# Performance work log

Measured on AMD Instinct MI355X. Metric: run time of the kernel, lower is better.

The kernel has to match this reference:

```python
import jax, jax.numpy as jnp
import numpy as np

KS, PH, PW, SH, SW = 3, 1, 1, 1, 1


def setup_inputs() -> dict:
    key = jax.random.key(0)
    k1, k2, k3 = jax.random.split(key, 3)
    bs, p_in, H, W = 8, 64, 64, 64
    p_out = 64
    vs = KS * KS + 1
    x = jax.random.normal(k1, (bs, p_in, H, W), dtype=jnp.float32)
    # kaiming-uniform-like init scale for filters (fan_in = p_in*vs*vs)
    fan_in = p_in * vs * vs
    bound = float(np.sqrt(6.0 / fan_in))
    filters = jax.random.uniform(k2, (p_out, p_in, vs, vs), dtype=jnp.float32,
                                 minval=-bound, maxval=bound)
    biases = jax.random.uniform(k3, (p_out,), dtype=jnp.float32, minval=-1.0, maxval=1.0)
    return {"x": x, "filters": filters, "biases": biases}


def reference(x, filters, biases):
    # x: (bs, p_in, H, W); filters: (p_out, p_in, vs, vs); biases: (p_out,)
    bs, p_in = x.shape[0], x.shape[1]
    p_out = filters.shape[0]
    vs = KS * KS + 1
    # Extract ks x ks patches -> (bs, p_in*ks*ks, Ho, Wo), feature dim ordered (C, kh, kw)
    patches = jax.lax.conv_general_dilated_patches(
        x, filter_shape=(KS, KS), window_strides=(SH, SW),
        padding=[(PH, PH), (PW, PW)])
    Ho, Wo = patches.shape[-2], patches.shape[-1]
    P = patches.reshape(bs, p_in, KS * KS, Ho, Wo)
    # Prepend constant 1 -> augmented patch vector s of length vs (matches torch cat(ones, spot))
    ones = jnp.ones((bs, p_in, 1, Ho, Wo), dtype=x.dtype)
    S = jnp.concatenate([ones, P], axis=2)            # (bs, p_in, vs, Ho, Wo)
    # Move pixels to a single leading dim: (M, p_in, vs) with M = bs*Ho*Wo
    S = S.transpose(0, 3, 4, 1, 2).reshape(bs * Ho * Wo, p_in, vs)
    # Per-pixel, per-channel outer product s s^T: (M, p_in, vs, vs)
    Q = S[:, :, :, None] * S[:, :, None, :]
    # Quadratic form contraction with filters as one GEMM:
    # out[m, o] = sum_{c,i,j} Q[m,c,i,j] * filters[o,c,i,j]
    out = Q.reshape(bs * Ho * Wo, p_in * vs * vs) @ filters.reshape(p_out, -1).T
    out = out + biases[None, :]
    return out.reshape(bs, Ho, Wo, p_out).transpose(0, 3, 1, 2)
```

## Files before the change

kernel.cpp:

```cpp
#include <hip/hip_runtime.h>
#include <stdint.h>

#define HH 64
#define WW 64
#define PIN 64
#define POUT 64
#define NFEAT 54
#define SEGB 16384
#define NSEG 27

typedef _Float16 half8 __attribute__((ext_vector_type(8)));
typedef _Float16 half4 __attribute__((ext_vector_type(4)));
typedef float f32x4 __attribute__((ext_vector_type(4)));
typedef float f32x16 __attribute__((ext_vector_type(16)));

__device__ constexpr int KT[54] = {0,0,0,0,0,0,0,0,0, 1,1,1,1,1,1,1,1,1, 2,2,2,2,2,2,2,2,
                                   3,3,3,3,3,3,3, 4,4,4,4,4,4, 5,5,5,5,5, 6,6,6,6, 7,7,7, 8,8, 9};
__device__ constexpr int LT[54] = {1,2,3,4,5,6,7,8,9, 1,2,3,4,5,6,7,8,9, 2,3,4,5,6,7,8,9,
                                   3,4,5,6,7,8,9, 4,5,6,7,8,9, 5,6,7,8,9, 6,7,8,9, 7,8,9, 8,9, 9};

__global__ __launch_bounds__(256) void prep_filters(
    const float* __restrict__ f, const float* __restrict__ bias,
    _Float16* __restrict__ fprep, float* __restrict__ fconst) {
    __shared__ float lds_f[6400];

    const int o = blockIdx.x;
    const int t = threadIdx.x;
    const float* fo = f + (size_t)o * 6400;

    for (int i = t; i < 6400; i += 256) lds_f[i] = fo[i];
    __syncthreads();

    if (t < 64) {
        float v = lds_f[t * 100];
        #pragma unroll
        for (int m = 32; m >= 1; m >>= 1) v += __shfl_xor(v, m, 64);
        if (t == 0) fconst[o] = bias[o] + v;
    }

    for (int q = t; q < NFEAT * 8; q += 256) {
        int feat = q >> 3;
        int cg = q & 7;
        int k = KT[feat], l = LT[feat];
        half8 chunk;
        #pragma unroll
        for (int jj = 0; jj < 8; ++jj) {
            const float* fc = lds_f + (cg * 8 + jj) * 100;
            float v;
            if (k == 0)      v = fc[l] + fc[l * 10];
            else if (k == l) v = fc[k * 10 + k];
            else             v = fc[k * 10 + l] + fc[l * 10 + k];
            chunk[jj] = (_Float16)v;
        }
        size_t byte = (size_t)feat * 8192 + (cg >> 1) * 2048 + (o >> 5) * 1024
                    + ((o & 31) + 32 * (cg & 1)) * 16;
        *(half8*)((char*)fprep + byte) = chunk;
    }
}

__global__ __launch_bounds__(512, 4) void poly2d_mfma(
    const float* __restrict__ x, const _Float16* __restrict__ fprep,
    const float* __restrict__ fconst, float* __restrict__ out)
{
    __shared__ __align__(16) char smB[2 * SEGB];
    __shared__ __align__(16) char smx[25344];

    const int t = threadIdx.x;
    const int lane = t & 63;
    const int wid = t >> 6;
    const int bid = (blockIdx.x & 7) * 64 + (blockIdx.x >> 3);
    const int b = bid >> 6;
    const int hrow = bid & 63;

#define STAGE(ss)                                                                         \
    do {                                                                                  \
        const char* s_ = (const char*)fprep + (size_t)(ss) * SEGB;                        \
        _Pragma("unroll")                                                                 \
        for (int r_ = 0; r_ < 2; ++r_)                                                    \
            __builtin_amdgcn_global_load_lds(                                             \
                (const __attribute__((address_space(1))) unsigned int*)(const void*)(s_ + r_ * 8192 + t * 16), \
                (__attribute__((address_space(3))) unsigned int*)(void*)(smB + ((ss) & 1) * SEGB + r_ * 8192 + (wid << 10)), \
                16, 0, 0);                                                                \
    } while (0)

    STAGE(0);
    STAGE(1);

    {
        const int w = t & 63;
        const int wl = w + 1;
        #pragma unroll
        for (int h = 0; h < 3; ++h) {
            int h_in = hrow - 1 + h;
            bool hok = ((unsigned)h_in < HH);
            #pragma unroll
            for (int cc = 0; cc < 2; ++cc) {
                int c = wid * 8 + cc * 4;
                float v0 = 0.f, v1 = 0.f, v2 = 0.f, v3 = 0.f;
                if (hok) {
                    const float* gx = x + (((size_t)b * PIN + c) * HH + h_in) * WW + w;
                    v0 = gx[0]; v1 = gx[4096]; v2 = gx[8192]; v3 = gx[12288];
                }
                half4 pk = {(_Float16)v0, (_Float16)v1, (_Float16)v2, (_Float16)v3};
                int byte = ((h * 66 + wl) * 8 + ((c >> 3) ^ (wl & 7))) * 16 + (c & 7) * 2;
                *(half4*)(smx + byte) = pk;
            }
        }
        if (t < 48) {
            int h = t >> 4, side = (t >> 3) & 1, cg = t & 7;
            int wl2 = side ? 65 : 0;
            int byte = ((h * 66 + wl2) * 8 + (cg ^ (wl2 & 7))) * 16;
            f32x4 z = {0.f, 0.f, 0.f, 0.f};
            *(f32x4*)(smx + byte) = z;
        }
    }
    __syncthreads();

    const int kc = wid >> 1;
    const int mwid = wid & 1;
    const int wbase = mwid * 32;
    const int l31 = lane & 31;
    const int lhi = lane >> 5;

    half8 xp[9];
    #pragma unroll
    for (int p = 1; p <= 9; ++p) {
        const int dh = (p - 1) / 3 - 1, dw = (p - 1) % 3 - 1;
        int wl = wbase + l31 + dw + 1;
        int hidx = dh + 1;
        int cgl = kc * 2 + lhi;
        int byte = ((hidx * 66 + wl) * 8 + (cgl ^ (wl & 7))) * 16;
        xp[p - 1] = *(const half8*)(smx + byte);
    }
    __syncthreads();

    f32x16 acc0 = {}, acc1 = {};
    const int boff = (kc << 11) + (lane << 4);

    #pragma unroll
    for (int s = 0; s < NSEG; ++s) {
        if (s == NSEG - 1) { asm volatile("s_waitcnt vmcnt(0)" ::: "memory"); }
        else               { asm volatile("s_waitcnt vmcnt(2)" ::: "memory"); }
        asm volatile("" ::: "memory");
        __builtin_amdgcn_s_barrier();
        asm volatile("" ::: "memory");

        const char* bseg = smB + (s & 1) * SEGB + boff;
        half8 Bb0[2], Bb1[2];
        #pragma unroll
        for (int j = 0; j < 2; ++j) {
            Bb0[j] = *(const half8*)(bseg + j * 8192);
            Bb1[j] = *(const half8*)(bseg + j * 8192 + 1024);
        }
        #pragma unroll
        for (int j = 0; j < 2; ++j) {
            const int f = s * 2 + j;
            const int k = KT[f], l = LT[f];
            half8 a = (k == 0) ? xp[l - 1] : xp[k - 1] * xp[l - 1];
            acc0 = __builtin_amdgcn_mfma_f32_32x32x16_f16(a, Bb0[j], acc0, 0, 0, 0);
            acc1 = __builtin_amdgcn_mfma_f32_32x32x16_f16(a, Bb1[j], acc1, 0, 0, 0);
        }

        asm volatile("s_waitcnt lgkmcnt(0)" ::: "memory");
        asm volatile("" ::: "memory");
        __builtin_amdgcn_s_barrier();
        asm volatile("" ::: "memory");
        if (s + 2 < NSEG) STAGE(s + 2);
    }
#undef STAGE

    __syncthreads();
    float* os = (float*)smx;

    #pragma unroll
    for (int pass = 0; pass < 4; ++pass) {
        if (kc == pass) {
            #pragma unroll
            for (int nb = 0; nb < 2; ++nb) {
                #pragma unroll
                for (int r = 0; r < 16; ++r) {
                    int row = (r & 3) + 8 * (r >> 2) + 4 * lhi;
                    int m = mwid * 32 + row;
                    int col = l31 + nb * 32;
                    float v = nb ? acc1[r] : acc0[r];
                    if (pass == 0) os[m * 65 + col] = v;
                    else           os[m * 65 + col] += v;
                }
            }
        }
        __syncthreads();
    }

    {
        const int w = t & 63;
        #pragma unroll
        for (int oo = 0; oo < 8; ++oo) {
            int o = wid * 8 + oo;
            float val = os[w * 65 + o] + fconst[o];
            out[(((size_t)b * POUT + o) * HH + hrow) * WW + w] = val;
        }
    }
}

__global__ __launch_bounds__(256) void poly2d_fp32(
    const float* __restrict__ x, const float* __restrict__ f,
    const float* __restrict__ bias, float* __restrict__ out)
{
    const int t = threadIdx.x;
    const int wo = t & 63;
    const int ho = (blockIdx.x & 15) * 4 + (t >> 6);
    const int o = (blockIdx.x >> 4) & 63;
    const int b = blockIdx.x >> 10;

    float acc = bias[o];
    const float* xb = x + (size_t)b * PIN * HH * WW;
    const float* fo = f + (size_t)o * PIN * 100;
    for (int c = 0; c < PIN; ++c) {
        const float* xc = xb + (size_t)c * HH * WW;
        float s[10];
        s[0] = 1.0f;
        #pragma unroll
        for (int kh = 0; kh < 3; ++kh) {
            int h = ho - 1 + kh;
            bool hok = ((unsigned)h < HH);
            #pragma unroll
            for (int kw = 0; kw < 3; ++kw) {
                int w = wo - 1 + kw;
                s[1 + kh * 3 + kw] = (hok && (unsigned)w < WW) ? xc[h * WW + w] : 0.0f;
            }
        }
        const float* fc = fo + c * 100;
        #pragma unroll
        for (int i = 0; i < 10; ++i) {
            float wsum = 0.0f;
            #pragma unroll
            for (int j = 0; j < 10; ++j) wsum = fmaf(fc[i * 10 + j], s[j], wsum);
            acc = fmaf(wsum, s[i], acc);
        }
    }
    out[(((size_t)b * POUT + o) * HH + ho) * WW + wo] = acc;
}

extern "C" void kernel_launch(void* const* d_in, const int* in_sizes, int n_in,
                              void* d_out, int out_size, void* d_ws, size_t ws_size,
                              hipStream_t stream) {
    const float* x    = (const float*)d_in[0];
    const float* filt = (const float*)d_in[1];
    const float* bias = (const float*)d_in[2];
    float* out = (float*)d_out;

    const size_t FPREP_BYTES = (size_t)NFEAT * POUT * PIN * 2;
    if (ws_size < FPREP_BYTES + 256) {
        poly2d_fp32<<<dim3(8 * 64 * 16), dim3(256), 0, stream>>>(x, filt, bias, out);
        return;
    }
    _Float16* fprep = (_Float16*)d_ws;
    float* fconst = (float*)((char*)d_ws + FPREP_BYTES);

    prep_filters<<<dim3(64), dim3(256), 0, stream>>>(filt, bias, fprep, fconst);
    poly2d_mfma<<<dim3(512), dim3(512), 0, stream>>>(x, fprep, fconst, out);
}
```

Before: 29.42 us.

## Process two output rows per block with 2x2 MFMA tiles and triple-buffered filters

Each block now computes two output rows (128 pixels) instead of one. Each wave holds two A tiles and four accumulators, so every filter segment staged into LDS is reused twice, and the total filter traffic from global memory is halved. The filter pipeline moves from double to triple buffering with adjusted vmcnt waits. Edge padding is now handled by clamping and zeroing rather than by padded LDS columns. In exchange the grid halves to 256 blocks, and more registers and LDS are used, which lowers occupancy (launch bounds 512,2) and may leave CUs underused on a 256-CU part.

Result: faster. 27.98 us (-4.9%).

```diff
diff --git a/kernel.cpp b/kernel.cpp
--- a/kernel.cpp
+++ b/kernel.cpp
@@ -58,19 +58,19 @@
     }
 }
 
-__global__ __launch_bounds__(512, 4) void poly2d_mfma(
+__global__ __launch_bounds__(512, 2) void poly2d_mfma(
     const float* __restrict__ x, const _Float16* __restrict__ fprep,
     const float* __restrict__ fconst, float* __restrict__ out)
 {
-    __shared__ __align__(16) char smB[2 * SEGB];
-    __shared__ __align__(16) char smx[25344];
+    __shared__ __align__(16) char smB[3 * SEGB];
+    __shared__ __align__(16) char smx[33792];
 
     const int t = threadIdx.x;
     const int lane = t & 63;
     const int wid = t >> 6;
-    const int bid = (blockIdx.x & 7) * 64 + (blockIdx.x >> 3);
-    const int b = bid >> 6;
-    const int hrow = bid & 63;
+    const int bid = (blockIdx.x & 7) * 32 + (blockIdx.x >> 3);
+    const int b = bid >> 5;
+    const int rp = bid & 31;
 
 #define STAGE(ss)                                                                         \
     do {                                                                                  \
@@ -79,19 +79,19 @@
         for (int r_ = 0; r_ < 2; ++r_)                                                    \
             __builtin_amdgcn_global_load_lds(                                             \
                 (const __attribute__((address_space(1))) unsigned int*)(const void*)(s_ + r_ * 8192 + t * 16), \
-                (__attribute__((address_space(3))) unsigned int*)(void*)(smB + ((ss) & 1) * SEGB + r_ * 8192 + (wid << 10)), \
+                (__attribute__((address_space(3))) unsigned int*)(void*)(smB + ((ss) % 3) * SEGB + r_ * 8192 + (wid << 10)), \
                 16, 0, 0);                                                                \
     } while (0)
 
     STAGE(0);
     STAGE(1);
+    STAGE(2);
 
     {
         const int w = t & 63;
-        const int wl = w + 1;
-        #pragma unroll
-        for (int h = 0; h < 3; ++h) {
-            int h_in = hrow - 1 + h;
+        #pragma unroll
+        for (int h = 0; h < 4; ++h) {
+            int h_in = rp * 2 - 1 + h;
             bool hok = ((unsigned)h_in < HH);
             #pragma unroll
             for (int cc = 0; cc < 2; ++cc) {
@@ -102,102 +102,110 @@
                     v0 = gx[0]; v1 = gx[4096]; v2 = gx[8192]; v3 = gx[12288];
                 }
                 half4 pk = {(_Float16)v0, (_Float16)v1, (_Float16)v2, (_Float16)v3};
-                int byte = ((h * 66 + wl) * 8 + ((c >> 3) ^ (wl & 7))) * 16 + (c & 7) * 2;
+                int byte = ((h * 64 + w) * 8 + ((c >> 3) ^ (w & 7))) * 16 + (c & 7) * 2;
                 *(half4*)(smx + byte) = pk;
             }
         }
-        if (t < 48) {
-            int h = t >> 4, side = (t >> 3) & 1, cg = t & 7;
-            int wl2 = side ? 65 : 0;
-            int byte = ((h * 66 + wl2) * 8 + (cg ^ (wl2 & 7))) * 16;
-            f32x4 z = {0.f, 0.f, 0.f, 0.f};
-            *(f32x4*)(smx + byte) = z;
-        }
     }
     __syncthreads();
 
     const int kc = wid >> 1;
-    const int mwid = wid & 1;
-    const int wbase = mwid * 32;
+    const int msup = wid & 1;
     const int l31 = lane & 31;
     const int lhi = lane >> 5;
 
-    half8 xp[9];
+    half8 xp[9][2];
     #pragma unroll
     for (int p = 1; p <= 9; ++p) {
         const int dh = (p - 1) / 3 - 1, dw = (p - 1) % 3 - 1;
-        int wl = wbase + l31 + dw + 1;
-        int hidx = dh + 1;
-        int cgl = kc * 2 + lhi;
-        int byte = ((hidx * 66 + wl) * 8 + (cgl ^ (wl & 7))) * 16;
-        xp[p - 1] = *(const half8*)(smx + byte);
-    }
-    __syncthreads();
-
-    f32x16 acc0 = {}, acc1 = {};
+        #pragma unroll
+        for (int mb = 0; mb < 2; ++mb) {
+            int wl = mb * 32 + l31 + dw;
+            int wc = wl < 0 ? 0 : (wl > 63 ? 63 : wl);
+            int hidx = msup + dh + 1;
+            int cgl = kc * 2 + lhi;
+            int byte = ((hidx * 64 + wc) * 8 + (cgl ^ (wc & 7))) * 16;
+            half8 v = *(const half8*)(smx + byte);
+            if ((unsigned)wl >= 64u) v = half8{};
+            xp[p - 1][mb] = v;
+        }
+    }
+    __syncthreads();
+
+    f32x16 acc00 = {}, acc01 = {}, acc10 = {}, acc11 = {};
     const int boff = (kc << 11) + (lane << 4);
 
     #pragma unroll
     for (int s = 0; s < NSEG; ++s) {
-        if (s == NSEG - 1) { asm volatile("s_waitcnt vmcnt(0)" ::: "memory"); }
-        else               { asm volatile("s_waitcnt vmcnt(2)" ::: "memory"); }
+        if (s < NSEG - 2)       { asm volatile("s_waitcnt vmcnt(4)" ::: "memory"); }
+        else if (s == NSEG - 2) { asm volatile("s_waitcnt vmcnt(2)" ::: "memory"); }
+        else                    { asm volatile("s_waitcnt vmcnt(0)" ::: "memory"); }
         asm volatile("" ::: "memory");
         __builtin_amdgcn_s_barrier();
         asm volatile("" ::: "memory");
 
-        const char* bseg = smB + (s & 1) * SEGB + boff;
-        half8 Bb0[2], Bb1[2];
+        const char* bseg = smB + (s % 3) * SEGB + boff;
         #pragma unroll
         for (int j = 0; j < 2; ++j) {
-            Bb0[j] = *(const half8*)(bseg + j * 8192);
-            Bb1[j] = *(const half8*)(bseg + j * 8192 + 1024);
-        }
-        #pragma unroll
-        for (int j = 0; j < 2; ++j) {
+            half8 b0 = *(const half8*)(bseg + j * 8192);
+            half8 b1 = *(const half8*)(bseg + j * 8192 + 1024);
             const int f = s * 2 + j;
             const int k = KT[f], l = LT[f];
-            half8 a = (k == 0) ? xp[l - 1] : xp[k - 1] * xp[l - 1];
-            acc0 = __builtin_amdgcn_mfma_f32_32x32x16_f16(a, Bb0[j], acc0, 0, 0, 0);
-            acc1 = __builtin_amdgcn_mfma_f32_32x32x16_f16(a, Bb1[j], acc1, 0, 0, 0);
+            half8 a0 = (k == 0) ? xp[l - 1][0] : xp[k - 1][0] * xp[l - 1][0];
+            half8 a1 = (k == 0) ? xp[l - 1][1] : xp[k - 1][1] * xp[l - 1][1];
+            acc00 = __builtin_amdgcn_mfma_f32_32x32x16_f16(a0, b0, acc00, 0, 0, 0);
+            acc01 = __builtin_amdgcn_mfma_f32_32x32x16_f16(a0, b1, acc01, 0, 0, 0);
+            acc10 = __builtin_amdgcn_mfma_f32_32x32x16_f16(a1, b0, acc10, 0, 0, 0);
+            acc11 = __builtin_amdgcn_mfma_f32_32x32x16_f16(a1, b1, acc11, 0, 0, 0);
         }
 
         asm volatile("s_waitcnt lgkmcnt(0)" ::: "memory");
         asm volatile("" ::: "memory");
         __builtin_amdgcn_s_barrier();
         asm volatile("" ::: "memory");
-        if (s + 2 < NSEG) STAGE(s + 2);
+        if (s + 3 < NSEG) STAGE(s + 3);
     }
 #undef STAGE
 
     __syncthreads();
     float* os = (float*)smx;
+
+#define EPI(ACC, MB, NB, OP)                                                              \
+    do {                                                                                  \
+        _Pragma("unroll")                                                                 \
+        for (int r = 0; r < 16; ++r) {                                                    \
+            int m = (r & 3) + 8 * (r >> 2) + 4 * lhi;                                     \
+            int px = msup * 64 + (MB) * 32 + m;                                           \
+            int col = l31 + (NB) * 32;                                                    \
+            os[px * 65 + col] OP (ACC)[r];                                                \
+        }                                                                                 \
+    } while (0)
 
     #pragma unroll
     for (int pass = 0; pass < 4; ++pass) {
         if (kc == pass) {
-            #pragma unroll
-            for (int nb = 0; nb < 2; ++nb) {
-                #pragma unroll
-                for (int r = 0; r < 16; ++r) {
-                    int row = (r & 3) + 8 * (r >> 2) + 4 * lhi;
-                    int m = mwid * 32 + row;
-                    int col = l31 + nb * 32;
-                    float v = nb ? acc1[r] : acc0[r];
-                    if (pass == 0) os[m * 65 + col] = v;
-                    else           os[m * 65 + col] += v;
-                }
+            if (pass == 0) {
+                EPI(acc00, 0, 0, =); EPI(acc01, 0, 1, =);
+                EPI(acc10, 1, 0, =); EPI(acc11, 1, 1, =);
+            } else {
+                EPI(acc00, 0, 0, +=); EPI(acc01, 0, 1, +=);
+                EPI(acc10, 1, 0, +=); EPI(acc11, 1, 1, +=);
             }
         }
         __syncthreads();
     }
+#undef EPI
 
     {
         const int w = t & 63;
         #pragma unroll
-        for (int oo = 0; oo < 8; ++oo) {
-            int o = wid * 8 + oo;
-            float val = os[w * 65 + o] + fconst[o];
-            out[(((size_t)b * POUT + o) * HH + hrow) * WW + w] = val;
+        for (int h2 = 0; h2 < 2; ++h2) {
+            #pragma unroll
+            for (int oo = 0; oo < 8; ++oo) {
+                int o = wid * 8 + oo;
+                float val = os[(h2 * 64 + w) * 65 + o] + fconst[o];
+                out[(((size_t)b * POUT + o) * HH + (rp * 2 + h2)) * WW + w] = val;
+            }
         }
     }
 }
@@ -258,5 +266,5 @@
     float* fconst = (float*)((char*)d_ws + FPREP_BYTES);
 
     prep_filters<<<dim3(64), dim3(256), 0, stream>>>(filt, bias, fprep, fconst);
-    poly2d_mfma<<<dim3(512), dim3(512), 0, stream>>>(x, fprep, fconst, out);
-}
+    poly2d_mfma<<<dim3(256), dim3(512), 0, stream>>>(x, fprep, fconst, out);
+}
```
